# Optimization experiments

Measured on AMD Instinct MI355X. Metric: run time of the kernel, lower is better.

The kernel has to match this reference:

```python
import jax, jax.numpy as jnp
import numpy as np

B, S, A, H = 32, 256, 6, 1024
OBS, GLOB, MASK, AGF = 520, 30, 52, 73
NTYPE = 5


def setup_inputs() -> dict:
    key = jax.random.key(0)
    ks = jax.random.split(key, 24)
    inputs = jax.random.normal(ks[0], (B, S, OBS), dtype=jnp.float32)
    # per-agent player-type lives at concat-column 1 -> raw column 30 + a*73 + 1
    types = jax.random.randint(ks[1], (B, A), 0, NTYPE).astype(jnp.float32)
    cols = np.array(GLOB + np.arange(A) * AGF + 1)
    inputs = inputs.at[:, :, cols].set(jnp.broadcast_to(types[:, None, :], (B, S, A)))
    # binary action mask in the last 52 columns
    mask = jax.random.bernoulli(ks[2], 0.7, (B, S, MASK)).astype(jnp.float32)
    inputs = inputs.at[:, :, -MASK:].set(mask)
    sc = 0.05
    p = {
        'inputs': inputs,
        'state0': jnp.zeros((B, A * H), dtype=jnp.float32),
        'W_emb': jax.random.normal(ks[3], (NTYPE, 102, 512)) * sc,
        'b_emb': jax.random.normal(ks[4], (NTYPE, 512)) * sc,
        'W_ih': jax.random.normal(ks[5], (3 * H, 512)) * sc,
        'W_hh': jax.random.normal(ks[6], (3 * H, H)) * sc,
        'b_ih': jax.random.normal(ks[7], (3 * H,)) * sc,
        'b_hh': jax.random.normal(ks[8], (3 * H,)) * sc,
        'Wg0': jax.random.normal(ks[9], (H, 4, 256)) * sc,
        'a0s': jax.random.normal(ks[10], (4, 256)) * sc,
        'a0d': jax.random.normal(ks[11], (4, 256)) * sc,
        'Wg1': jax.random.normal(ks[12], (H, 4, 256)) * sc,
        'a1s': jax.random.normal(ks[13], (4, 256)) * sc,
        'a1d': jax.random.normal(ks[14], (4, 256)) * sc,
        'Wa1': jax.random.normal(ks[15], (NTYPE, H, 512)) * sc,
        'ba1': jax.random.normal(ks[16], (NTYPE, 512)) * sc,
        'Wa2': jax.random.normal(ks[17], (NTYPE, 512, 52)) * sc,
        'ba2': jax.random.normal(ks[18], (NTYPE, 52)) * sc,
    }
    return p


def _gat(x, W, a_s, a_d):
    # x: [B, N, F]; standard multi-head GAT over the fully-connected agent graph
    hf = jnp.einsum('bnf,fhd->bnhd', x, W)
    src = jnp.einsum('bnhd,hd->bhn', hf, a_s)
    dst = jnp.einsum('bnhd,hd->bhn', hf, a_d)
    e = jax.nn.leaky_relu(src[:, :, :, None] + dst[:, :, None, :], 0.2)  # [b,h,i,j]
    att = jax.nn.softmax(e, axis=-1)
    out = jnp.einsum('bhij,bjhd->bihd', att, hf)
    return jax.nn.elu(out.reshape(x.shape[0], x.shape[1], -1))


def reference(inputs, state0, W_emb, b_emb, W_ih, W_hh, b_ih, b_hh,
              Wg0, a0s, a0d, Wg1, a1s, a1d, Wa1, ba1, Wa2, ba2):
    b, s, _ = inputs.shape
    masks = inputs[:, :, -MASK:]
    glob = inputs[:, :, :GLOB]
    agent = inputs[:, :, GLOB:-MASK].reshape(b, s, A, AGF)
    x = jnp.concatenate([agent, jnp.broadcast_to(glob[:, :, None, :], (b, s, A, GLOB))], -1)
    x = x.transpose(0, 2, 1, 3).reshape(b * A, s, AGF + GLOB)  # [N, S, 103]
    vec = x[:, :, 1:]                                           # [N, S, 102]
    types = vec[:, 0, 0].astype(jnp.int32)                      # per-agent player type
    # type-routed Linear + ReLU (grouped GEMM instead of the python loop)
    emb = jax.nn.relu(jnp.einsum('nsf,nfd->nsd', vec, W_emb[types]) + b_emb[types][:, None, :])
    # single-layer GRU, batched over all B*A agents
    xg = emb @ W_ih.T + b_ih                                    # [N, S, 3H]
    h0 = state0.reshape(b * A, H)

    def step(h, xt):
        hg = h @ W_hh.T + b_hh
        xr, xz, xn = jnp.split(xt, 3, axis=-1)
        hr, hz, hn = jnp.split(hg, 3, axis=-1)
        r = jax.nn.sigmoid(xr + hr)
        z = jax.nn.sigmoid(xz + hz)
        n = jnp.tanh(xn + r * hn)
        return (1.0 - z) * n + z * h, None

    hT, _ = jax.lax.scan(step, h0, xg.transpose(1, 0, 2))       # final hidden == last output
    g0 = _gat(hT.reshape(b, A, H), Wg0, a0s, a0d)
    g1 = _gat(g0, Wg1, a1s, a1d)
    f0 = g1[:, 0, :]                                            # agent-0 features [B, 1024]
    pt = types.reshape(b, A)[:, 0]                              # per-sample routing type
    h1 = jax.nn.relu(jnp.einsum('bf,bfd->bd', f0, Wa1[pt]) + ba1[pt])
    logits = jnp.einsum('bf,bfd->bd', h1, Wa2[pt]) + ba2[pt]    # [B, 52]
    logits = logits[:, None, :]                                 # [B, 1, 52]
    action_logit = jnp.where(masks != 0, logits, jnp.zeros_like(logits))  # broadcast -> [B, S, 52]
    return action_logit, hT
```

## Files before the change

kernel.cpp:

```cpp
#include <hip/hip_runtime.h>
#include <hip/hip_bf16.h>
#include <cmath>

#define BB    32
#define SS    256
#define AA    6
#define HH    1024
#define OBSF  520
#define GLOBF 30
#define MASKF 52
#define AGFF  73
#define NSEQ  192
#define EMBD  512

#define GRID_GRU 256
#define THR_GRU  192
#define LDS_W_BYTES (48*3*64*16)

typedef short bf16x8 __attribute__((ext_vector_type(8)));
typedef float f32x4  __attribute__((ext_vector_type(4)));

__device__ __forceinline__ float sigmoidf_(float x){ return 1.f/(1.f + expf(-x)); }
__device__ __forceinline__ short f2bf(float x){
    __hip_bfloat16 h = __float2bfloat16(x);
    return *reinterpret_cast<short*>(&h);
}

__device__ __forceinline__ bf16x8 load_bypass16(const short* p){
    union { unsigned long long u[2]; bf16x8 v; } x;
    x.u[0] = __hip_atomic_load((const unsigned long long*)p,     __ATOMIC_RELAXED, __HIP_MEMORY_SCOPE_AGENT);
    x.u[1] = __hip_atomic_load((const unsigned long long*)(p+4), __ATOMIC_RELAXED, __HIP_MEMORY_SCOPE_AGENT);
    return x.v;
}

__global__ __launch_bounds__(256) void cvt_bf16(
    const float* __restrict__ in, __hip_bfloat16* __restrict__ out, int n)
{
    for (int i = blockIdx.x*256 + threadIdx.x; i < n; i += gridDim.x*256)
        out[i] = __float2bfloat16(in[i]);
}

__global__ __launch_bounds__(256) void emb_kernel(
    const float* __restrict__ inp, const float* __restrict__ W_emb,
    const float* __restrict__ b_emb, __hip_bfloat16* __restrict__ emb)
{
    const int n  = blockIdx.x;
    const int s0 = blockIdx.y * 16;
    const int b  = n / AA, a = n % AA;
    const int tid = threadIdx.x;
    const int ty = (int)inp[(size_t)(b*SS)*OBSF + GLOBF + a*AGFF + 1];

    __shared__ float vecs[16][102];
    for (int idx = tid; idx < 16*102; idx += 256) {
        int ss = idx / 102, f = idx % 102;
        int g  = f + 1;
        int col = (g < AGFF) ? (GLOBF + a*AGFF + g) : (g - AGFF);
        vecs[ss][f] = inp[((size_t)(b*SS + s0 + ss))*OBSF + col];
    }
    __syncthreads();

    float acc0[16], acc1[16];
    #pragma unroll
    for (int ss = 0; ss < 16; ++ss) { acc0[ss] = 0.f; acc1[ss] = 0.f; }

    const float* Wb = W_emb + (size_t)ty*102*EMBD;
    for (int f = 0; f < 102; ++f) {
        float w0 = Wb[f*EMBD + tid];
        float w1 = Wb[f*EMBD + tid + 256];
        #pragma unroll
        for (int ss = 0; ss < 16; ++ss) {
            float v = vecs[ss][f];
            acc0[ss] += v * w0;
            acc1[ss] += v * w1;
        }
    }
    float bb0 = b_emb[ty*EMBD + tid], bb1 = b_emb[ty*EMBD + tid + 256];
    for (int ss = 0; ss < 16; ++ss) {
        __hip_bfloat16* o = emb + ((size_t)n*SS + s0 + ss)*EMBD;
        o[tid]       = __float2bfloat16(fmaxf(acc0[ss] + bb0, 0.f));
        o[tid + 256] = __float2bfloat16(fmaxf(acc1[ss] + bb1, 0.f));
    }
}

__global__ __launch_bounds__(THR_GRU, 1) void gru_persistent(
    const float* __restrict__ state0,
    const short* __restrict__ emb_bf,
    const short* __restrict__ Whh_bf, const short* __restrict__ Wih_bf,
    const float* __restrict__ b_ih, const float* __restrict__ b_hh,
    short* __restrict__ hbf0, short* __restrict__ hbf1,
    float* __restrict__ hT_out, unsigned* __restrict__ bar)
{
    extern __shared__ short ldsW[];
    __shared__ short ldsH[3*256];
    const int tid = threadIdx.x, wave = tid >> 6, lane = tid & 63;
    const int nt = blockIdx.x & 63, mg = blockIdx.x >> 6;
    const int i0 = nt*16, mt = mg*3 + wave;
    const int col = lane & 15, rgrp = lane >> 4;
    const int n = i0 + col;
    unsigned* flags = bar + mg*64;

    for (int idx = tid; idx < 32*3*64; idx += THR_GRU) {
        int l = idx & 63, g = (idx >> 6) % 3, kt = idx / 192;
        const short* src = Whh_bf + ((size_t)(g*HH + i0 + (l & 15)))*HH + kt*32 + (l >> 4)*8;
        *(bf16x8*)(ldsW + (size_t)idx*8) = *(const bf16x8*)src;
    }
    short* ldsW2 = ldsW + 32*3*64*8;
    for (int idx = tid; idx < 16*3*64; idx += THR_GRU) {
        int l = idx & 63, g = (idx >> 6) % 3, kt = idx / 192;
        const short* src = Wih_bf + ((size_t)(g*HH + i0 + (l & 15)))*EMBD + kt*32 + (l >> 4)*8;
        *(bf16x8*)(ldsW2 + (size_t)idx*8) = *(const bf16x8*)src;
    }

    float hreg[4];
    #pragma unroll
    for (int r_ = 0; r_ < 4; ++r_) {
        hreg[r_] = state0[(size_t)(mt*16 + rgrp*4 + r_)*HH + n];
        ldsH[wave*256 + (rgrp*4 + r_)*16 + col] = f2bf(hreg[r_]);
    }
    __syncthreads();
    {
        int w2 = tid >> 6, rem = tid & 63, rr = rem >> 2, cg = rem & 3;
        unsigned long long v = *(const unsigned long long*)(ldsH + w2*256 + rr*16 + cg*4);
        __hip_atomic_store((unsigned long long*)(hbf0 + (size_t)((mg*3 + w2)*16 + rr)*HH + i0 + cg*4),
                           v, __ATOMIC_RELAXED, __HIP_MEMORY_SCOPE_AGENT);
    }
    asm volatile("s_waitcnt vmcnt(0)" ::: "memory");
    __syncthreads();
    if (tid == 0)
        __hip_atomic_store(&flags[nt], 1u, __ATOMIC_RELAXED, __HIP_MEMORY_SCOPE_AGENT);

    const float bir = b_ih[n], biz = b_ih[HH+n], bin_ = b_ih[2*HH+n];
    const float bhr = b_hh[n], bhz = b_hh[HH+n], bhn  = b_hh[2*HH+n];

    const size_t lane_h_off = (size_t)(mt*16 + col)*HH + rgrp*8;
    const size_t lane_e_off = (size_t)(mt*16 + col)*SS*EMBD + rgrp*8;

    f32x4 ax0 = {0.f,0.f,0.f,0.f}, ax1 = ax0, ax3 = ax0;
    {
        const short* Ae = emb_bf + lane_e_off;
        #pragma unroll 8
        for (int kt = 0; kt < 16; ++kt) {
            bf16x8 a  = *(const bf16x8*)(Ae + kt*32);
            bf16x8 b0 = *(const bf16x8*)(ldsW2 + ((kt*3 + 0)*64 + lane)*8);
            bf16x8 b1 = *(const bf16x8*)(ldsW2 + ((kt*3 + 1)*64 + lane)*8);
            bf16x8 b2 = *(const bf16x8*)(ldsW2 + ((kt*3 + 2)*64 + lane)*8);
            ax0 = __builtin_amdgcn_mfma_f32_16x16x32_bf16(a, b0, ax0, 0,0,0);
            ax1 = __builtin_amdgcn_mfma_f32_16x16x32_bf16(a, b1, ax1, 0,0,0);
            ax3 = __builtin_amdgcn_mfma_f32_16x16x32_bf16(a, b2, ax3, 0,0,0);
        }
    }
    if (wave == 0) {
        for (;;) {
            unsigned f = __hip_atomic_load(&flags[lane], __ATOMIC_RELAXED, __HIP_MEMORY_SCOPE_AGENT);
            if (__ballot(f >= 1u) == ~0ull) break;
            __builtin_amdgcn_s_sleep(1);
        }
    }
    __syncthreads();

    for (int s = 0; s < SS; ++s) {
        const short* cur = (s & 1) ? hbf1 : hbf0;
        short*       nxt = (s & 1) ? hbf0 : hbf1;

        const short* Ah = cur + lane_h_off;
        bf16x8 fa[32];
        #pragma unroll
        for (int j = 0; j < 32; ++j) fa[j] = load_bypass16(Ah + j*32);

        f32x4 a0 = ax0, a1 = ax1, a2 = {0.f,0.f,0.f,0.f};
        #pragma unroll
        for (int kt = 0; kt < 32; ++kt) {
            bf16x8 b0 = *(const bf16x8*)(ldsW + ((kt*3 + 0)*64 + lane)*8);
            bf16x8 b1 = *(const bf16x8*)(ldsW + ((kt*3 + 1)*64 + lane)*8);
            bf16x8 b2 = *(const bf16x8*)(ldsW + ((kt*3 + 2)*64 + lane)*8);
            a0 = __builtin_amdgcn_mfma_f32_16x16x32_bf16(fa[kt], b0, a0, 0,0,0);
            a1 = __builtin_amdgcn_mfma_f32_16x16x32_bf16(fa[kt], b1, a1, 0,0,0);
            a2 = __builtin_amdgcn_mfma_f32_16x16x32_bf16(fa[kt], b2, a2, 0,0,0);
        }

        #pragma unroll
        for (int r_ = 0; r_ < 4; ++r_) {
            float r  = sigmoidf_(a0[r_] + bir + bhr);
            float z  = sigmoidf_(a1[r_] + biz + bhz);
            float nn = tanhf(ax3[r_] + bin_ + r*(a2[r_] + bhn));
            float hv = (1.f - z)*nn + z*hreg[r_];
            hreg[r_] = hv;
            ldsH[wave*256 + (rgrp*4 + r_)*16 + col] = f2bf(hv);
        }

        if (s < SS-1) {
            __syncthreads();
            {
                int w2 = tid >> 6, rem = tid & 63, rr = rem >> 2, cg = rem & 3;
                unsigned long long v = *(const unsigned long long*)(ldsH + w2*256 + rr*16 + cg*4);
                __hip_atomic_store((unsigned long long*)(nxt + (size_t)((mg*3 + w2)*16 + rr)*HH + i0 + cg*4),
                                   v, __ATOMIC_RELAXED, __HIP_MEMORY_SCOPE_AGENT);
            }
            asm volatile("s_waitcnt vmcnt(0)" ::: "memory");
            __syncthreads();
            if (tid == 0)
                __hip_atomic_store(&flags[nt], (unsigned)(s + 2), __ATOMIC_RELAXED, __HIP_MEMORY_SCOPE_AGENT);

            ax0 = (f32x4){0.f,0.f,0.f,0.f}; ax1 = ax0; ax3 = ax0;
            const short* Ae = emb_bf + lane_e_off + (size_t)(s+1)*EMBD;
            #pragma unroll 8
            for (int kt = 0; kt < 16; ++kt) {
                bf16x8 a  = *(const bf16x8*)(Ae + kt*32);
                bf16x8 b0 = *(const bf16x8*)(ldsW2 + ((kt*3 + 0)*64 + lane)*8);
                bf16x8 b1 = *(const bf16x8*)(ldsW2 + ((kt*3 + 1)*64 + lane)*8);
                bf16x8 b2 = *(const bf16x8*)(ldsW2 + ((kt*3 + 2)*64 + lane)*8);
                ax0 = __builtin_amdgcn_mfma_f32_16x16x32_bf16(a, b0, ax0, 0,0,0);
                ax1 = __builtin_amdgcn_mfma_f32_16x16x32_bf16(a, b1, ax1, 0,0,0);
                ax3 = __builtin_amdgcn_mfma_f32_16x16x32_bf16(a, b2, ax3, 0,0,0);
            }
            {
                unsigned target = (unsigned)(s + 2);
                if (wave == 0) {
                    for (;;) {
                        unsigned f = __hip_atomic_load(&flags[lane], __ATOMIC_RELAXED, __HIP_MEMORY_SCOPE_AGENT);
                        if (__ballot(f >= target) == ~0ull) break;
                        __builtin_amdgcn_s_sleep(1);
                    }
                }
            }
            __syncthreads();
        }
    }

    #pragma unroll
    for (int r_ = 0; r_ < 4; ++r_)
        hT_out[(size_t)(mt*16 + rgrp*4 + r_)*HH + n] = hreg[r_];
}

__global__ __launch_bounds__(256) void gru_step_mfma(
    const float* __restrict__ h_in, const __hip_bfloat16* __restrict__ h_in_bf,
    float* __restrict__ h_out, __hip_bfloat16* __restrict__ h_out_bf,
    const __hip_bfloat16* __restrict__ emb_bf,
    const __hip_bfloat16* __restrict__ Whh_bf, const __hip_bfloat16* __restrict__ Wih_bf,
    const float* __restrict__ b_ih, const float* __restrict__ b_hh, int s)
{
    const int i0   = blockIdx.x * 16;
    const int tid  = threadIdx.x;
    const int wave = tid >> 6, lane = tid & 63;
    const int col  = lane & 15, rgrp = lane >> 4;
    const int n    = i0 + col;
    const int kofs = rgrp * 8;

    f32x4 acc[3][4];
    #pragma unroll
    for (int mi = 0; mi < 3; ++mi)
        #pragma unroll
        for (int g = 0; g < 4; ++g) acc[mi][g] = (f32x4){0.f,0.f,0.f,0.f};

    {
        const short* Ab = (const short*)h_in_bf;
        const short* B0 = (const short*)Whh_bf + ((size_t)(      n))*HH + kofs;
        const short* B1 = (const short*)Whh_bf + ((size_t)(HH  + n))*HH + kofs;
        const short* B2 = (const short*)Whh_bf + ((size_t)(2*HH+ n))*HH + kofs;
        #pragma unroll 2
        for (int kt = 0; kt < 32; ++kt) {
            const int kk = kt * 32;
            bf16x8 b0 = *(const bf16x8*)(B0 + kk);
            bf16x8 b1 = *(const bf16x8*)(B1 + kk);
            bf16x8 b2 = *(const bf16x8*)(B2 + kk);
            #pragma unroll
            for (int mi = 0; mi < 3; ++mi) {
                const int m = (wave*3 + mi)*16 + col;
                bf16x8 a = *(const bf16x8*)(Ab + (size_t)m*HH + kk + kofs);
                acc[mi][0] = __builtin_amdgcn_mfma_f32_16x16x32_bf16(a, b0, acc[mi][0], 0,0,0);
                acc[mi][1] = __builtin_amdgcn_mfma_f32_16x16x32_bf16(a, b1, acc[mi][1], 0,0,0);
                acc[mi][2] = __builtin_amdgcn_mfma_f32_16x16x32_bf16(a, b2, acc[mi][2], 0,0,0);
            }
        }
    }
    {
        const short* Ab = (const short*)emb_bf;
        const short* B0 = (const short*)Wih_bf + ((size_t)(      n))*EMBD + kofs;
        const short* B1 = (const short*)Wih_bf + ((size_t)(HH  + n))*EMBD + kofs;
        const short* B2 = (const short*)Wih_bf + ((size_t)(2*HH+ n))*EMBD + kofs;
        #pragma unroll 2
        for (int kt = 0; kt < 16; ++kt) {
            const int kk = kt * 32;
            bf16x8 b0 = *(const bf16x8*)(B0 + kk);
            bf16x8 b1 = *(const bf16x8*)(B1 + kk);
            bf16x8 b2 = *(const bf16x8*)(B2 + kk);
            #pragma unroll
            for (int mi = 0; mi < 3; ++mi) {
                const int m = (wave*3 + mi)*16 + col;
                bf16x8 a = *(const bf16x8*)(Ab + ((size_t)m*SS + s)*EMBD + kk + kofs);
                acc[mi][0] = __builtin_amdgcn_mfma_f32_16x16x32_bf16(a, b0, acc[mi][0], 0,0,0);
                acc[mi][1] = __builtin_amdgcn_mfma_f32_16x16x32_bf16(a, b1, acc[mi][1], 0,0,0);
                acc[mi][3] = __builtin_amdgcn_mfma_f32_16x16x32_bf16(a, b2, acc[mi][3], 0,0,0);
            }
        }
    }
    const float bir = b_ih[n], biz = b_ih[HH + n], bin_ = b_ih[2*HH + n];
    const float bhr = b_hh[n], bhz = b_hh[HH + n], bhn  = b_hh[2*HH + n];
    #pragma unroll
    for (int mi = 0; mi < 3; ++mi) {
        #pragma unroll
        for (int r_ = 0; r_ < 4; ++r_) {
            const int m = (wave*3 + mi)*16 + rgrp*4 + r_;
            float r  = sigmoidf_(acc[mi][0][r_] + bir + bhr);
            float z  = sigmoidf_(acc[mi][1][r_] + biz + bhz);
            float nn = tanhf(acc[mi][3][r_] + bin_ + r*(acc[mi][2][r_] + bhn));
            const size_t idx = (size_t)m*HH + n;
            float hv = (1.f - z)*nn + z*h_in[idx];
            h_out[idx]    = hv;
            h_out_bf[idx] = __float2bfloat16(hv);
        }
    }
}

__global__ __launch_bounds__(256) void sgemm_rrr(
    const float* __restrict__ A, const float* __restrict__ B,
    float* __restrict__ C, int M, int N, int K)
{
    const int n0 = blockIdx.x * 64;
    const int m0 = blockIdx.y * 64;
    const int tid = threadIdx.x;
    const int tn = tid & 15, tm = tid >> 4;

    __shared__ float As[16][68];
    __shared__ float Bs[16][68];
    float acc[4][4];
    #pragma unroll
    for (int i = 0; i < 4; ++i)
        #pragma unroll
        for (int j = 0; j < 4; ++j) acc[i][j] = 0.f;

    for (int k0 = 0; k0 < K; k0 += 16) {
        {
            int ml = tid >> 2, k4 = (tid & 3) << 2;
            float4 av = *(const float4*)(A + (size_t)(m0 + ml)*K + k0 + k4);
            As[k4 + 0][ml] = av.x; As[k4 + 1][ml] = av.y;
            As[k4 + 2][ml] = av.z; As[k4 + 3][ml] = av.w;
            int kl = tid >> 4, n4 = (tid & 15) << 2;
            *(float4*)&Bs[kl][n4] = *(const float4*)(B + (size_t)(k0 + kl)*N + n0 + n4);
        }
        __syncthreads();
        #pragma unroll
        for (int kk = 0; kk < 16; ++kk) {
            float4 a4 = *(float4*)&As[kk][tm << 2];
            float4 b4 = *(float4*)&Bs[kk][tn << 2];
            acc[0][0] += a4.x*b4.x; acc[0][1] += a4.x*b4.y; acc[0][2] += a4.x*b4.z; acc[0][3] += a4.x*b4.w;
            acc[1][0] += a4.y*b4.x; acc[1][1] += a4.y*b4.y; acc[1][2] += a4.y*b4.z; acc[1][3] += a4.y*b4.w;
            acc[2][0] += a4.z*b4.x; acc[2][1] += a4.z*b4.y; acc[2][2] += a4.z*b4.z; acc[2][3] += a4.z*b4.w;
            acc[3][0] += a4.w*b4.x; acc[3][1] += a4.w*b4.y; acc[3][2] += a4.w*b4.z; acc[3][3] += a4.w*b4.w;
        }
        __syncthreads();
    }
    #pragma unroll
    for (int qm = 0; qm < 4; ++qm) {
        float4 v = make_float4(acc[qm][0], acc[qm][1], acc[qm][2], acc[qm][3]);
        *(float4*)(C + (size_t)(m0 + tm*4 + qm)*N + n0 + tn*4) = v;
    }
}

__global__ __launch_bounds__(256) void gat_att(
    const float* __restrict__ hf, const float* __restrict__ a_s,
    const float* __restrict__ a_d, float* __restrict__ gout)
{
    const int b = blockIdx.x;
    const int tid = threadIdx.x;
    __shared__ float hfs[6][1024];
    __shared__ float srcs[24], dsts[24];
    __shared__ float att[4][36];

    for (int idx = tid; idx < 6*1024; idx += 256)
        hfs[idx >> 10][idx & 1023] = hf[(size_t)b*6144 + idx];
    __syncthreads();

    const int w = tid >> 6, lane = tid & 63;
    for (int p = w; p < 24; p += 4) {
        int h = p / 6, nn = p % 6;
        float as_ = 0.f, ad_ = 0.f;
        for (int c = lane; c < 256; c += 64) {
            float v = hfs[nn][h*256 + c];
            as_ += v * a_s[h*256 + c];
            ad_ += v * a_d[h*256 + c];
        }
        #pragma unroll
        for (int off = 32; off; off >>= 1) {
            as_ += __shfl_down(as_, off);
            ad_ += __shfl_down(ad_, off);
        }
        if (lane == 0) { srcs[p] = as_; dsts[p] = ad_; }
    }
    __syncthreads();

    if (tid < 24) {
        int h = tid / 6, i = tid % 6;
        float e[6], mx = -1e30f;
        #pragma unroll
        for (int j = 0; j < 6; ++j) {
            float x = srcs[h*6 + i] + dsts[h*6 + j];
            e[j] = (x >= 0.f) ? x : 0.2f*x;
            mx = fmaxf(mx, e[j]);
        }
        float sum = 0.f;
        #pragma unroll
        for (int j = 0; j < 6; ++j) { e[j] = expf(e[j] - mx); sum += e[j]; }
        float inv = 1.f / sum;
        #pragma unroll
        for (int j = 0; j < 6; ++j) att[h][i*6 + j] = e[j]*inv;
    }
    __syncthreads();

    for (int idx = tid; idx < 6144; idx += 256) {
        int i = idx >> 10, hd = idx & 1023, h = hd >> 8;
        float v = 0.f;
        #pragma unroll
        for (int j = 0; j < 6; ++j) v += att[h][i*6 + j] * hfs[j][hd];
        gout[(size_t)b*6144 + idx] = (v > 0.f) ? v : (expf(v) - 1.f);
    }
}

__global__ __launch_bounds__(256) void head_kernel(
    const float* __restrict__ g1, const float* __restrict__ inp,
    const float* __restrict__ Wa1, const float* __restrict__ ba1,
    const float* __restrict__ Wa2, const float* __restrict__ ba2,
    float* __restrict__ out)
{
    const int b = blockIdx.x;
    const int tid = threadIdx.x;
    const int pt = (int)inp[(size_t)b*SS*OBSF + GLOBF + 1];

    __shared__ float f0s[1024];
    __shared__ float h1s[512];
    __shared__ float lgs[52];

    for (int idx = tid; idx < 1024; idx += 256) f0s[idx] = g1[(size_t)b*6144 + idx];
    __syncthreads();
    {
        float acc0 = 0.f, acc1 = 0.f;
        const float* W = Wa1 + (size_t)pt*1024*512;
        for (int f = 0; f < 1024; ++f) {
            float v = f0s[f];
            acc0 += v * W[f*512 + tid];
            acc1 += v * W[f*512 + tid + 256];
        }
        h1s[tid]       = fmaxf(acc0 + ba1[pt*512 + tid], 0.f);
        h1s[tid + 256] = fmaxf(acc1 + ba1[pt*512 + tid + 256], 0.f);
    }
    __syncthreads();
    if (tid < 52) {
        float acc = 0.f;
        const float* W = Wa2 + (size_t)pt*512*52;
        for (int f = 0; f < 512; ++f) acc += h1s[f] * W[f*52 + tid];
        lgs[tid] = acc + ba2[pt*52 + tid];
    }
    __syncthreads();
    for (int idx = tid; idx < SS*MASKF; idx += 256) {
        int s = idx / MASKF, c = idx % MASKF;
        float mv = inp[((size_t)b*SS + s)*OBSF + (OBSF - MASKF) + c];
        out[(size_t)b*SS*MASKF + idx] = (mv != 0.f) ? lgs[c] : 0.f;
    }
}

extern "C" void kernel_launch(void* const* d_in, const int* in_sizes, int n_in,
                              void* d_out, int out_size, void* d_ws, size_t ws_size,
                              hipStream_t stream)
{
    const float* inp    = (const float*)d_in[0];
    const float* state0 = (const float*)d_in[1];
    const float* W_emb  = (const float*)d_in[2];
    const float* b_emb  = (const float*)d_in[3];
    const float* W_ih   = (const float*)d_in[4];
    const float* W_hh   = (const float*)d_in[5];
    const float* b_ih   = (const float*)d_in[6];
    const float* b_hh   = (const float*)d_in[7];
    const float* Wg0    = (const float*)d_in[8];
    const float* a0s    = (const float*)d_in[9];
    const float* a0d    = (const float*)d_in[10];
    const float* Wg1    = (const float*)d_in[11];
    const float* a1s    = (const float*)d_in[12];
    const float* a1d    = (const float*)d_in[13];
    const float* Wa1    = (const float*)d_in[14];
    const float* ba1    = (const float*)d_in[15];
    const float* Wa2    = (const float*)d_in[16];
    const float* ba2    = (const float*)d_in[17];
    float* out = (float*)d_out;

    char* p = (char*)d_ws;
    __hip_bfloat16* emb_bf = (__hip_bfloat16*)p;  p += (size_t)NSEQ*SS*EMBD*2;
    __hip_bfloat16* Whh_bf = (__hip_bfloat16*)p;  p += (size_t)3*HH*HH*2;
    __hip_bfloat16* Wih_bf = (__hip_bfloat16*)p;  p += (size_t)3*HH*EMBD*2;
    float* hb0 = (float*)p;                       p += (size_t)NSEQ*HH*4;
    float* hb1 = (float*)p;                       p += (size_t)NSEQ*HH*4;
    short* hbf0 = (short*)p;                      p += (size_t)NSEQ*HH*2;
    short* hbf1 = (short*)p;                      p += (size_t)NSEQ*HH*2;
    float* hf = (float*)p;                        p += (size_t)NSEQ*HH*4;
    float* g0 = (float*)p;                        p += (size_t)NSEQ*HH*4;
    float* g1 = (float*)p;                        p += (size_t)NSEQ*HH*4;
    unsigned* bar = (unsigned*)p;                 p += 4096;
    if (ws_size < (size_t)(p - (char*)d_ws)) return;

    cvt_bf16<<<512, 256, 0, stream>>>(W_hh, Whh_bf, 3*HH*HH);
    cvt_bf16<<<512, 256, 0, stream>>>(W_ih, Wih_bf, 3*HH*EMBD);

    emb_kernel<<<dim3(NSEQ, 16), 256, 0, stream>>>(inp, W_emb, b_emb, emb_bf);

    hipMemsetAsync(bar, 0, 4096, stream);
    float* hT_out = out + (size_t)BB*SS*MASKF;

    static int attr_set = 0;
    if (!attr_set) {
        hipFuncSetAttribute((const void*)gru_persistent,
                            hipFuncAttributeMaxDynamicSharedMemorySize, LDS_W_BYTES);
        attr_set = 1;
    }
    const short* emb_bf_s = (const short*)emb_bf;
    const short* Whh_bf_s = (const short*)Whh_bf;
    const short* Wih_bf_s = (const short*)Wih_bf;
    void* args[] = { (void*)&state0, (void*)&emb_bf_s, (void*)&Whh_bf_s, (void*)&Wih_bf_s,
                     (void*)&b_ih, (void*)&b_hh, (void*)&hbf0, (void*)&hbf1,
                     (void*)&hT_out, (void*)&bar };
    hipError_t e = hipLaunchCooperativeKernel((const void*)gru_persistent,
                                              dim3(GRID_GRU), dim3(THR_GRU),
                                              args, LDS_W_BYTES, stream);
    const float* hT;
    if (e == hipSuccess) {
        hT = hT_out;
    } else {
        cvt_bf16<<<192, 256, 0, stream>>>(state0, (__hip_bfloat16*)hbf0, NSEQ*HH);
        hipMemcpyAsync(hb0, state0, (size_t)NSEQ*HH*4, hipMemcpyDeviceToDevice, stream);
        float* hf32[2] = {hb0, hb1};
        short* hbf[2] = {hbf0, hbf1};
        for (int s = 0; s < SS; ++s) {
            gru_step_mfma<<<64, 256, 0, stream>>>(
                hf32[s & 1], (const __hip_bfloat16*)hbf[s & 1],
                hf32[(s + 1) & 1], (__hip_bfloat16*)hbf[(s + 1) & 1],
                (const __hip_bfloat16*)emb_bf, Whh_bf, Wih_bf, b_ih, b_hh, s);
        }
        hT = hb0;
        hipMemcpyAsync(hT_out, hb0, (size_t)NSEQ*HH*4, hipMemcpyDeviceToDevice, stream);
    }

    sgemm_rrr<<<dim3(16, 3), 256, 0, stream>>>(hT, Wg0, hf, NSEQ, HH, HH);
    gat_att<<<BB, 256, 0, stream>>>(hf, a0s, a0d, g0);
    sgemm_rrr<<<dim3(16, 3), 256, 0, stream>>>(g0, Wg1, hf, NSEQ, HH, HH);
    gat_att<<<BB, 256, 0, stream>>>(hf, a1s, a1d, g1);

    head_kernel<<<BB, 256, 0, stream>>>(g1, inp, Wa1, ba1, Wa2, ba2, out);
}
```

Baseline: 3.202 ms.

## Rotate GRU hidden-state buffers over 64 slots to allow cached loads

The GRU hidden state now cycles through 64 distinct address slots instead of two ping-pong buffers. Each step's fresh addresses let the kernel read h with ordinary vector loads instead of cache-bypassing atomic loads, with an acquire fence only every 32 steps. This is meant to cut per-step load latency and instruction count in the persistent recurrent loop. It relies on stale cache lines never being hit within the fence window, a subtle memory-ordering assumption that also costs a much larger workspace.

```diff
diff --git a/kernel.cpp b/kernel.cpp
--- a/kernel.cpp
+++ b/kernel.cpp
@@ -16,6 +16,9 @@
 #define GRID_GRU 256
 #define THR_GRU  192
 #define LDS_W_BYTES (48*3*64*16)
+#define HSLOT 196608
+#define NROT  64
+#define INVP  32
 
 typedef short bf16x8 __attribute__((ext_vector_type(8)));
 typedef float f32x4  __attribute__((ext_vector_type(4)));
@@ -24,13 +27,6 @@
 __device__ __forceinline__ short f2bf(float x){
     __hip_bfloat16 h = __float2bfloat16(x);
     return *reinterpret_cast<short*>(&h);
-}
-
-__device__ __forceinline__ bf16x8 load_bypass16(const short* p){
-    union { unsigned long long u[2]; bf16x8 v; } x;
-    x.u[0] = __hip_atomic_load((const unsigned long long*)p,     __ATOMIC_RELAXED, __HIP_MEMORY_SCOPE_AGENT);
-    x.u[1] = __hip_atomic_load((const unsigned long long*)(p+4), __ATOMIC_RELAXED, __HIP_MEMORY_SCOPE_AGENT);
-    return x.v;
 }
 
 __global__ __launch_bounds__(256) void cvt_bf16(
@@ -87,7 +83,7 @@
     const short* __restrict__ emb_bf,
     const short* __restrict__ Whh_bf, const short* __restrict__ Wih_bf,
     const float* __restrict__ b_ih, const float* __restrict__ b_hh,
-    short* __restrict__ hbf0, short* __restrict__ hbf1,
+    short* __restrict__ hbase,
     float* __restrict__ hT_out, unsigned* __restrict__ bar)
 {
     extern __shared__ short ldsW[];
@@ -121,7 +117,7 @@
     {
         int w2 = tid >> 6, rem = tid & 63, rr = rem >> 2, cg = rem & 3;
         unsigned long long v = *(const unsigned long long*)(ldsH + w2*256 + rr*16 + cg*4);
-        __hip_atomic_store((unsigned long long*)(hbf0 + (size_t)((mg*3 + w2)*16 + rr)*HH + i0 + cg*4),
+        __hip_atomic_store((unsigned long long*)(hbase + (size_t)((mg*3 + w2)*16 + rr)*HH + i0 + cg*4),
                            v, __ATOMIC_RELAXED, __HIP_MEMORY_SCOPE_AGENT);
     }
     asm volatile("s_waitcnt vmcnt(0)" ::: "memory");
@@ -159,13 +155,17 @@
     __syncthreads();
 
     for (int s = 0; s < SS; ++s) {
-        const short* cur = (s & 1) ? hbf1 : hbf0;
-        short*       nxt = (s & 1) ? hbf0 : hbf1;
+        if ((s & (INVP-1)) == 0)
+            __builtin_amdgcn_fence(__ATOMIC_ACQUIRE, "agent");
+        asm volatile("" ::: "memory");
+
+        const short* cur = hbase + (size_t)(s & (NROT-1))*HSLOT;
+        short*       nxt = hbase + (size_t)((s+1) & (NROT-1))*HSLOT;
 
         const short* Ah = cur + lane_h_off;
         bf16x8 fa[32];
         #pragma unroll
-        for (int j = 0; j < 32; ++j) fa[j] = load_bypass16(Ah + j*32);
+        for (int j = 0; j < 32; ++j) fa[j] = *(const bf16x8*)(Ah + j*32);
 
         f32x4 a0 = ax0, a1 = ax1, a2 = {0.f,0.f,0.f,0.f};
         #pragma unroll
@@ -486,15 +486,17 @@
     __hip_bfloat16* emb_bf = (__hip_bfloat16*)p;  p += (size_t)NSEQ*SS*EMBD*2;
     __hip_bfloat16* Whh_bf = (__hip_bfloat16*)p;  p += (size_t)3*HH*HH*2;
     __hip_bfloat16* Wih_bf = (__hip_bfloat16*)p;  p += (size_t)3*HH*EMBD*2;
-    float* hb0 = (float*)p;                       p += (size_t)NSEQ*HH*4;
-    float* hb1 = (float*)p;                       p += (size_t)NSEQ*HH*4;
-    short* hbf0 = (short*)p;                      p += (size_t)NSEQ*HH*2;
-    short* hbf1 = (short*)p;                      p += (size_t)NSEQ*HH*2;
-    float* hf = (float*)p;                        p += (size_t)NSEQ*HH*4;
-    float* g0 = (float*)p;                        p += (size_t)NSEQ*HH*4;
-    float* g1 = (float*)p;                        p += (size_t)NSEQ*HH*4;
     unsigned* bar = (unsigned*)p;                 p += 4096;
+    short* hbase = (short*)p;                     p += (size_t)NROT*HSLOT*2;
     if (ws_size < (size_t)(p - (char*)d_ws)) return;
+
+    short* hbf0 = hbase;
+    short* hbf1 = hbase + (size_t)HSLOT;
+    float* hb0  = (float*)(hbase + (size_t)2*HSLOT);
+    float* hb1  = (float*)(hbase + (size_t)4*HSLOT);
+    float* hf   = (float*)(hbase + (size_t)6*HSLOT);
+    float* g0   = (float*)(hbase + (size_t)8*HSLOT);
+    float* g1   = (float*)(hbase + (size_t)10*HSLOT);
 
     cvt_bf16<<<512, 256, 0, stream>>>(W_hh, Whh_bf, 3*HH*HH);
     cvt_bf16<<<512, 256, 0, stream>>>(W_ih, Wih_bf, 3*HH*EMBD);
@@ -514,7 +516,7 @@
     const short* Whh_bf_s = (const short*)Whh_bf;
     const short* Wih_bf_s = (const short*)Wih_bf;
     void* args[] = { (void*)&state0, (void*)&emb_bf_s, (void*)&Whh_bf_s, (void*)&Wih_bf_s,
-                     (void*)&b_ih, (void*)&b_hh, (void*)&hbf0, (void*)&hbf1,
+                     (void*)&b_ih, (void*)&b_hh, (void*)&hbase,
                      (void*)&hT_out, (void*)&bar };
     hipError_t e = hipLaunchCooperativeKernel((const void*)gru_persistent,
                                               dim3(GRID_GRU), dim3(THR_GRU),
```

After: 3.059 ms. -4.5%, faster.
